# Kernel optimization log

Measured on AMD Instinct MI355X. Metric: run time of the kernel, lower is better.

The kernel has to match this reference:

```python
import jax, jax.numpy as jnp
import numpy as np

N, D, E = 50000, 128, 800000
BN_EPS = 1e-3  # keras BatchNormalization default


def _ffn_block(x, g, b, m, v, W, bias):
    # BatchNorm (inference) -> Dropout (identity at inference) -> Dense + exact GELU
    xn = (x - m) * g * jax.lax.rsqrt(v + BN_EPS) + b
    return jax.nn.gelu(xn @ W + bias, approximate=False)


def setup_inputs() -> dict:
    key = jax.random.key(0)
    ks = jax.random.split(key, 24)
    inp = {
        "node_reps": jax.random.normal(ks[0], (N, D), dtype=jnp.float32),
        "edges": jax.random.randint(ks[1], (2, E), 0, N, dtype=jnp.int32),
        "edge_weights": jax.random.uniform(ks[2], (E,), dtype=jnp.float32),
    }
    def bn(i, dim):
        return (jax.random.normal(ks[i], (dim,)) * 0.1 + 1.0,   # gamma
                jax.random.normal(ks[i + 1], (dim,)) * 0.1,      # beta
                jax.random.normal(ks[i + 2], (dim,)) * 0.1,      # moving mean
                jax.random.uniform(ks[i + 3], (dim,)) + 0.5)     # moving var (>0)
    # prepare FFN: two blocks, D->D then D->D
    inp["pre_bn1_g"], inp["pre_bn1_b"], inp["pre_bn1_m"], inp["pre_bn1_v"] = bn(3, D)
    inp["pre_w1"] = jax.random.normal(ks[7], (D, D)) * (1.0 / np.sqrt(D))
    inp["pre_b1"] = jnp.zeros((D,), jnp.float32)
    inp["pre_bn2_g"], inp["pre_bn2_b"], inp["pre_bn2_m"], inp["pre_bn2_v"] = bn(8, D)
    inp["pre_w2"] = jax.random.normal(ks[12], (D, D)) * (1.0 / np.sqrt(D))
    inp["pre_b2"] = jnp.zeros((D,), jnp.float32)
    # update FFN: concat -> 2D input, then D->D
    inp["upd_bn1_g"], inp["upd_bn1_b"], inp["upd_bn1_m"], inp["upd_bn1_v"] = bn(13, 2 * D)
    inp["upd_w1"] = jax.random.normal(ks[17], (2 * D, D)) * (1.0 / np.sqrt(2 * D))
    inp["upd_b1"] = jnp.zeros((D,), jnp.float32)
    inp["upd_bn2_g"], inp["upd_bn2_b"], inp["upd_bn2_m"], inp["upd_bn2_v"] = bn(18, D)
    inp["upd_w2"] = jax.random.normal(ks[22], (D, D)) * (1.0 / np.sqrt(D))
    inp["upd_b2"] = jnp.zeros((D,), jnp.float32)
    return inp


def reference(node_reps, edges, edge_weights,
              pre_bn1_g, pre_bn1_b, pre_bn1_m, pre_bn1_v, pre_w1, pre_b1,
              pre_bn2_g, pre_bn2_b, pre_bn2_m, pre_bn2_v, pre_w2, pre_b2,
              upd_bn1_g, upd_bn1_b, upd_bn1_m, upd_bn1_v, upd_w1, upd_b1,
              upd_bn2_g, upd_bn2_b, upd_bn2_m, upd_bn2_v, upd_w2, upd_b2):
    num_nodes = node_reps.shape[0]
    node_idx, nbr_idx = edges[0], edges[1]
    # gather neighbour representations [E, D]
    nbr = jnp.take(node_reps, nbr_idx, axis=0)
    # prepare: FFN then scale by edge weights
    msg = _ffn_block(nbr, pre_bn1_g, pre_bn1_b, pre_bn1_m, pre_bn1_v, pre_w1, pre_b1)
    msg = _ffn_block(msg, pre_bn2_g, pre_bn2_b, pre_bn2_m, pre_bn2_v, pre_w2, pre_b2)
    msg = msg * edge_weights[:, None]
    # aggregate: segment_sum scatter back to nodes [N, D]
    agg = jax.ops.segment_sum(msg, node_idx, num_segments=num_nodes)
    # update: concat + FFN, then L2 normalize
    h = jnp.concatenate([node_reps, agg], axis=-1)  # [N, 2D]
    out = _ffn_block(h, upd_bn1_g, upd_bn1_b, upd_bn1_m, upd_bn1_v, upd_w1, upd_b1)
    out = _ffn_block(out, upd_bn2_g, upd_bn2_b, upd_bn2_m, upd_bn2_v, upd_w2, upd_b2)
    out = out * jax.lax.rsqrt(jnp.maximum(jnp.sum(out * out, axis=-1, keepdims=True), 1e-12))
    return out
```

## Files before the change

kernel.cpp:

```cpp
#include <hip/hip_runtime.h>
#include <hip/hip_bf16.h>
#include <math.h>

#define NN 50000
#define DD 128
#define EE 800000

static constexpr float BN_EPS = 1e-3f;

typedef __attribute__((ext_vector_type(8))) short bf16x8;
typedef __attribute__((ext_vector_type(4))) float f32x4;

#define MFMA16(a, b, c) __builtin_amdgcn_mfma_f32_16x16x32_bf16((a), (b), (c), 0, 0, 0)

__device__ __forceinline__ float gelu_f(float x) {
    float ax = fabsf(x) * 0.7071067811865475f;
    float t = __builtin_amdgcn_rcpf(fmaf(0.3275911f, ax, 1.0f));
    float p = t * fmaf(t, fmaf(t, fmaf(t, fmaf(t, 1.061405429f, -1.453152027f),
                                       1.421413741f), -0.284496736f), 0.254829592f);
    float e = __expf(-ax * ax);
    float er = fmaf(-p, e, 1.0f);
    float s = copysignf(er, x);
    return 0.5f * x * (1.0f + s);
}

__device__ __forceinline__ ushort f2bf_rn(float f) {
    uint u = __float_as_uint(f);
    return (ushort)((u + 0x7FFFu + ((u >> 16) & 1u)) >> 16);
}
__device__ __forceinline__ float bf2f(ushort h) {
    return __uint_as_float(((uint)h) << 16);
}

__device__ __forceinline__ uint pk2(float a, float b) {
    __hip_bfloat162 t = __float22bfloat162_rn(make_float2(a, b));
    uint r;
    __builtin_memcpy(&r, &t, 4);
    return r;
}

__device__ __forceinline__ void cvt_hilo(float4 x0, float4 x1, bf16x8& h, bf16x8& l) {
    float f[8] = {x0.x, x0.y, x0.z, x0.w, x1.x, x1.y, x1.z, x1.w};
    union U { uint u[4]; bf16x8 v; } uh, ul;
    #pragma unroll
    for (int j = 0; j < 4; ++j) {
        uint p = pk2(f[2 * j], f[2 * j + 1]);
        uh.u[j] = p;
        float h0 = __uint_as_float(p << 16);
        float h1 = __uint_as_float(p & 0xFFFF0000u);
        ul.u[j] = pk2(f[2 * j] - h0, f[2 * j + 1] - h1);
    }
    h = uh.v;
    l = ul.v;
}

__device__ __forceinline__ void pack_one(const float* __restrict__ W, const float* __restrict__ g,
                                         const float* __restrict__ v, ushort* __restrict__ hi,
                                         ushort* __restrict__ lo, int K, int idx) {
    int k = idx >> 7, col = idx & 127;
    float s = g[k] * rsqrtf(v[k] + BN_EPS);
    float f = s * W[idx];
    int S = K >> 5;
    int st = k >> 5, gq = (k >> 3) & 3, j = k & 7;
    int c = col >> 4, ln = (gq << 4) | (col & 15);
    int o = ((c * S + st) * 64 + ln) * 8 + j;
    ushort hb = f2bf_rn(f);
    hi[o] = hb;
    lo[o] = f2bf_rn(f - bf2f(hb));
}

__global__ void pack_all(
    const float* __restrict__ w1, const float* __restrict__ g1, const float* __restrict__ v1,
    ushort* __restrict__ W1h, ushort* __restrict__ W1l,
    const float* __restrict__ w2, const float* __restrict__ g2, const float* __restrict__ v2,
    ushort* __restrict__ W2h, ushort* __restrict__ W2l,
    const float* __restrict__ u1, const float* __restrict__ g3, const float* __restrict__ v3,
    ushort* __restrict__ U1h, ushort* __restrict__ U1l,
    const float* __restrict__ u2, const float* __restrict__ g4, const float* __restrict__ v4,
    ushort* __restrict__ U2h, ushort* __restrict__ U2l)
{
    int idx = blockIdx.x * 256 + threadIdx.x;
    if (idx < 16384)       pack_one(w1, g1, v1, W1h, W1l, 128, idx);
    else if (idx < 32768)  pack_one(w2, g2, v2, W2h, W2l, 128, idx - 16384);
    else if (idx < 65536)  pack_one(u1, g3, v3, U1h, U1l, 256, idx - 32768);
    else                   pack_one(u2, g4, v4, U2h, U2l, 128, idx - 65536);
}

__global__ void init_bias(const float* __restrict__ b1, const float* __restrict__ b2,
                          const float* __restrict__ ub1, const float* __restrict__ ub2,
                          float* __restrict__ B1f, float* __restrict__ B2f,
                          float* __restrict__ C1f, float* __restrict__ C2f) {
    int t = threadIdx.x;
    B1f[t] = b1[t]; B2f[t] = b2[t]; C1f[t] = ub1[t]; C2f[t] = ub2[t];
}

__global__ __launch_bounds__(256) void fold_all(
    const float* __restrict__ w1, const float* __restrict__ g1, const float* __restrict__ b1,
    const float* __restrict__ m1, const float* __restrict__ v1, float* __restrict__ B1f,
    const float* __restrict__ w2, const float* __restrict__ g2, const float* __restrict__ b2,
    const float* __restrict__ m2, const float* __restrict__ v2, float* __restrict__ B2f,
    const float* __restrict__ u1, const float* __restrict__ g3, const float* __restrict__ b3,
    const float* __restrict__ m3, const float* __restrict__ v3, float* __restrict__ C1f,
    const float* __restrict__ u2, const float* __restrict__ g4, const float* __restrict__ b4,
    const float* __restrict__ m4, const float* __restrict__ v4, float* __restrict__ C2f,
    int* __restrict__ cnt, int* __restrict__ spillCnt)
{
    for (int i = blockIdx.x * 256 + threadIdx.x; i < NN + 1; i += 20 * 256) {
        if (i < NN) cnt[i] = 0; else spillCnt[0] = 0;
    }

    const int rs = blockIdx.x * 32;
    const float *W, *g, *bb, *m, *v;
    float* bf;
    int k0;
    if (rs < 128)      { W = w1; g = g1; bb = b1; m = m1; v = v1; bf = B1f; k0 = rs; }
    else if (rs < 256) { W = w2; g = g2; bb = b2; m = m2; v = v2; bf = B2f; k0 = rs - 128; }
    else if (rs < 512) { W = u1; g = g3; bb = b3; m = m3; v = v3; bf = C1f; k0 = rs - 256; }
    else               { W = u2; g = g4; bb = b4; m = m4; v = v4; bf = C2f; k0 = rs - 512; }

    const int t = threadIdx.x, j = t & 127, h = t >> 7;
    float acc = 0.f;
    #pragma unroll
    for (int kk = 0; kk < 16; ++kk) {
        int k = k0 + h * 16 + kk;
        float s = g[k] * rsqrtf(v[k] + BN_EPS);
        float tt = bb[k] - m[k] * s;
        acc = fmaf(tt, W[k * DD + j], acc);
    }
    __shared__ float S[256];
    S[t] = acc;
    __syncthreads();
    if (h == 0) atomicAdd(&bf[j], S[j] + S[128 + j]);
}

#define YLD 136
#define BCAP 56
#define SPILL_CAP 100000
#define NCHUNK 400
#define CHSZ (EE / NCHUNK)
#define PSZ 6250
#define FILLB (NCHUNK * 8)

__global__ __launch_bounds__(512, 4) void prep_fill(
    const float* __restrict__ reps, const int* __restrict__ edges,
    const ushort* __restrict__ W1h, const ushort* __restrict__ W1l, const float* __restrict__ B1,
    const ushort* __restrict__ W2h, const ushort* __restrict__ W2l, const float* __restrict__ B2,
    ushort* __restrict__ msgN,
    int* __restrict__ cnt, int* __restrict__ spillCnt,
    int* __restrict__ spill, int* __restrict__ bucket)
{
    __shared__ ushort Yh[128 * YLD];

    if (blockIdx.x < FILLB) {
        const int part = blockIdx.x & 7;
        const int ch   = blockIdx.x >> 3;
        const int lo = part * PSZ, hi2 = lo + PSZ;
        const int base = ch * CHSZ;
        for (int i = threadIdx.x; i < CHSZ; i += 512) {
            int e = base + i;
            int d = edges[e];
            if (d >= lo && d < hi2) {
                int s = atomicAdd(&cnt[d], 1);
                if (s < BCAP) bucket[d * BCAP + s] = e;
                else { int sl = atomicAdd(spillCnt, 1); if (sl < SPILL_CAP) spill[sl] = e; }
            }
        }
        return;
    }

    const int pb = blockIdx.x - FILLB;
    if (pb >= 391) return;
    const int t = threadIdx.x;
    const int w = t >> 6, l = t & 63, lg = l >> 4, lr = l & 15;
    const int n0 = pb * 128;
    int n = n0 + w * 16 + lr;
    int nc = n < NN ? n : NN - 1;
    const float* src = reps + (size_t)nc * DD;

    float b1v[8], b2v[8];
    #pragma unroll
    for (int c = 0; c < 8; ++c) { b1v[c] = B1[c * 16 + lr]; b2v[c] = B2[c * 16 + lr]; }

    f32x4 acc[8];
    #pragma unroll
    for (int c = 0; c < 8; ++c) acc[c] = (f32x4)(0.f);

    #pragma unroll
    for (int s = 0; s < 4; ++s) {
        float4 x0 = *reinterpret_cast<const float4*>(src + s * 32 + lg * 8);
        float4 x1 = *reinterpret_cast<const float4*>(src + s * 32 + lg * 8 + 4);
        bf16x8 ah, al;
        cvt_hilo(x0, x1, ah, al);
        #pragma unroll
        for (int c = 0; c < 8; ++c) {
            bf16x8 bh = *reinterpret_cast<const bf16x8*>(W1h + (size_t)((c * 4 + s) * 64 + l) * 8);
            bf16x8 bl = *reinterpret_cast<const bf16x8*>(W1l + (size_t)((c * 4 + s) * 64 + l) * 8);
            acc[c] = MFMA16(al, bh, acc[c]);
            acc[c] = MFMA16(ah, bl, acc[c]);
            acc[c] = MFMA16(ah, bh, acc[c]);
        }
    }
    #pragma unroll
    for (int c = 0; c < 8; ++c) {
        #pragma unroll
        for (int i = 0; i < 4; ++i) {
            float yv = gelu_f(acc[c][i] + b1v[c]);
            Yh[(w * 16 + lg * 4 + i) * YLD + c * 16 + lr] = f2bf_rn(yv);
        }
    }

    #pragma unroll
    for (int c = 0; c < 8; ++c) acc[c] = (f32x4)(0.f);
    const ushort* yr = Yh + (w * 16 + lr) * YLD;
    #pragma unroll
    for (int s = 0; s < 4; ++s) {
        bf16x8 ah = *reinterpret_cast<const bf16x8*>(yr + s * 32 + lg * 8);
        #pragma unroll
        for (int c = 0; c < 8; ++c) {
            bf16x8 bh = *reinterpret_cast<const bf16x8*>(W2h + (size_t)((c * 4 + s) * 64 + l) * 8);
            bf16x8 bl = *reinterpret_cast<const bf16x8*>(W2l + (size_t)((c * 4 + s) * 64 + l) * 8);
            acc[c] = MFMA16(ah, bl, acc[c]);
            acc[c] = MFMA16(ah, bh, acc[c]);
        }
    }

    const int nrow = n0 + w * 16 + lg * 4;
    #pragma unroll
    for (int i = 0; i < 4; ++i) {
        if (nrow + i < NN) {
            #pragma unroll
            for (int c = 0; c < 8; ++c)
                msgN[(size_t)(nrow + i) * DD + c * 16 + lr] = f2bf_rn(gelu_f(acc[c][i] + b2v[c]));
        }
    }
}

__global__ __launch_bounds__(512, 8) void agg_node(
    const float* __restrict__ reps, const int* __restrict__ edges, const float* __restrict__ ew,
    const int* __restrict__ bucket, const int* __restrict__ cnt,
    const int* __restrict__ spillCnt, const int* __restrict__ spill,
    const ushort* __restrict__ msgN,
    const ushort* __restrict__ U1h, const ushort* __restrict__ U1l, const float* __restrict__ C1,
    const ushort* __restrict__ U2h, const ushort* __restrict__ U2l, const float* __restrict__ C2,
    float* __restrict__ out)
{
    __shared__ ushort aggL[64 * YLD];
    __shared__ ushort Yh[64 * YLD];
    __shared__ float ssqP[2][64];
    const int t = threadIdx.x;
    const int n0 = blockIdx.x * 64;

    {
        const int g = t >> 4, la = t & 15;
        const ushort* base = msgN + la * 8;
        #pragma unroll
        for (int it = 0; it < 2; ++it) {
            const int nl = g * 2 + it;
            const int node = n0 + nl;
            float acc[8] = {0.f, 0.f, 0.f, 0.f, 0.f, 0.f, 0.f, 0.f};
            if (node < NN) {
                const int dc = cnt[node];
                const int deg = dc < BCAP ? dc : BCAP;
                const int* b = bucket + node * BCAP;
                int k = 0;
                for (; k + 3 < deg; k += 4) {
                    int e0 = b[k], e1 = b[k + 1], e2 = b[k + 2], e3 = b[k + 3];
                    int q0 = edges[EE + e0], q1 = edges[EE + e1];
                    int q2 = edges[EE + e2], q3 = edges[EE + e3];
                    float w0 = ew[e0], w1 = ew[e1], w2 = ew[e2], w3 = ew[e3];
                    bf16x8 m0 = *reinterpret_cast<const bf16x8*>(base + (size_t)q0 * DD);
                    bf16x8 m1 = *reinterpret_cast<const bf16x8*>(base + (size_t)q1 * DD);
                    bf16x8 m2 = *reinterpret_cast<const bf16x8*>(base + (size_t)q2 * DD);
                    bf16x8 m3 = *reinterpret_cast<const bf16x8*>(base + (size_t)q3 * DD);
                    #pragma unroll
                    for (int j = 0; j < 8; ++j) {
                        acc[j] = fmaf(w0, bf2f((ushort)m0[j]), acc[j]);
                        acc[j] = fmaf(w1, bf2f((ushort)m1[j]), acc[j]);
                        acc[j] = fmaf(w2, bf2f((ushort)m2[j]), acc[j]);
                        acc[j] = fmaf(w3, bf2f((ushort)m3[j]), acc[j]);
                    }
                }
                for (; k < deg; ++k) {
                    int e0 = b[k];
                    int q0 = edges[EE + e0];
                    float w0 = ew[e0];
                    bf16x8 m0 = *reinterpret_cast<const bf16x8*>(base + (size_t)q0 * DD);
                    #pragma unroll
                    for (int j = 0; j < 8; ++j) acc[j] = fmaf(w0, bf2f((ushort)m0[j]), acc[j]);
                }
                if (dc > BCAP) {
                    int sc = spillCnt[0]; if (sc > SPILL_CAP) sc = SPILL_CAP;
                    for (int i = 0; i < sc; ++i) {
                        int eid = spill[i];
                        if (edges[eid] == node) {
                            int q0 = edges[EE + eid];
                            float w0 = ew[eid];
                            bf16x8 m0 = *reinterpret_cast<const bf16x8*>(base + (size_t)q0 * DD);
                            #pragma unroll
                            for (int j = 0; j < 8; ++j)
                                acc[j] = fmaf(w0, bf2f((ushort)m0[j]), acc[j]);
                        }
                    }
                }
            }
            uint4 o;
            o.x = pk2(acc[0], acc[1]);
            o.y = pk2(acc[2], acc[3]);
            o.z = pk2(acc[4], acc[5]);
            o.w = pk2(acc[6], acc[7]);
            *reinterpret_cast<uint4*>(&aggL[nl * YLD + la * 8]) = o;
        }
    }
    __syncthreads();

    const int w = t >> 6, l = t & 63, lg = l >> 4, lr = l & 15;
    const int wr = w & 3, hh = w >> 2;
    int n = n0 + wr * 16 + lr;
    int nc = n < NN ? n : NN - 1;

    float c1v[4], c2v[4];
    #pragma unroll
    for (int cc = 0; cc < 4; ++cc) {
        c1v[cc] = C1[(4 * hh + cc) * 16 + lr];
        c2v[cc] = C2[(4 * hh + cc) * 16 + lr];
    }

    f32x4 acc[4];
    #pragma unroll
    for (int cc = 0; cc < 4; ++cc) acc[cc] = (f32x4)(0.f);

    #pragma unroll
    for (int s = 0; s < 4; ++s) {
        const float* sp = reps + (size_t)nc * DD + s * 32 + lg * 8;
        float4 x0 = *reinterpret_cast<const float4*>(sp);
        float4 x1 = *reinterpret_cast<const float4*>(sp + 4);
        bf16x8 ah, al;
        cvt_hilo(x0, x1, ah, al);
        #pragma unroll
        for (int cc = 0; cc < 4; ++cc) {
            int c = 4 * hh + cc;
            bf16x8 bh = *reinterpret_cast<const bf16x8*>(U1h + (size_t)((c * 8 + s) * 64 + l) * 8);
            bf16x8 bl = *reinterpret_cast<const bf16x8*>(U1l + (size_t)((c * 8 + s) * 64 + l) * 8);
            acc[cc] = MFMA16(al, bh, acc[cc]);
            acc[cc] = MFMA16(ah, bl, acc[cc]);
            acc[cc] = MFMA16(ah, bh, acc[cc]);
        }
    }
    const ushort* ar = aggL + (wr * 16 + lr) * YLD;
    #pragma unroll
    for (int s = 4; s < 8; ++s) {
        bf16x8 ah = *reinterpret_cast<const bf16x8*>(ar + (s - 4) * 32 + lg * 8);
        #pragma unroll
        for (int cc = 0; cc < 4; ++cc) {
            int c = 4 * hh + cc;
            bf16x8 bh = *reinterpret_cast<const bf16x8*>(U1h + (size_t)((c * 8 + s) * 64 + l) * 8);
            bf16x8 bl = *reinterpret_cast<const bf16x8*>(U1l + (size_t)((c * 8 + s) * 64 + l) * 8);
            acc[cc] = MFMA16(ah, bl, acc[cc]);
            acc[cc] = MFMA16(ah, bh, acc[cc]);
        }
    }
    #pragma unroll
    for (int cc = 0; cc < 4; ++cc) {
        #pragma unroll
        for (int i = 0; i < 4; ++i) {
            float yv = gelu_f(acc[cc][i] + c1v[cc]);
            Yh[(wr * 16 + lg * 4 + i) * YLD + (4 * hh + cc) * 16 + lr] = f2bf_rn(yv);
        }
    }
    __syncthreads();

    #pragma unroll
    for (int cc = 0; cc < 4; ++cc) acc[cc] = (f32x4)(0.f);
    const ushort* yr2 = Yh + (wr * 16 + lr) * YLD;
    #pragma unroll
    for (int s = 0; s < 4; ++s) {
        bf16x8 ah = *reinterpret_cast<const bf16x8*>(yr2 + s * 32 + lg * 8);
        #pragma unroll
        for (int cc = 0; cc < 4; ++cc) {
            int c = 4 * hh + cc;
            bf16x8 bh = *reinterpret_cast<const bf16x8*>(U2h + (size_t)((c * 4 + s) * 64 + l) * 8);
            bf16x8 bl = *reinterpret_cast<const bf16x8*>(U2l + (size_t)((c * 4 + s) * 64 + l) * 8);
            acc[cc] = MFMA16(ah, bl, acc[cc]);
            acc[cc] = MFMA16(ah, bh, acc[cc]);
        }
    }

    float ssq[4] = {0.f, 0.f, 0.f, 0.f};
    #pragma unroll
    for (int cc = 0; cc < 4; ++cc) {
        #pragma unroll
        for (int i = 0; i < 4; ++i) {
            float vv = gelu_f(acc[cc][i] + c2v[cc]);
            acc[cc][i] = vv;
            ssq[i] = fmaf(vv, vv, ssq[i]);
        }
    }
    #pragma unroll
    for (int i = 0; i < 4; ++i) {
        #pragma unroll
        for (int msk = 1; msk < 16; msk <<= 1) ssq[i] += __shfl_xor(ssq[i], msk);
    }
    const int row0 = wr * 16 + lg * 4;
    if (lr == 0) {
        #pragma unroll
        for (int i = 0; i < 4; ++i) ssqP[hh][row0 + i] = ssq[i];
    }
    __syncthreads();
    #pragma unroll
    for (int i = 0; i < 4; ++i) {
        float tot = ssqP[0][row0 + i] + ssqP[1][row0 + i];
        float sc = rsqrtf(fmaxf(tot, 1e-12f));
        if (n0 + row0 + i < NN) {
            #pragma unroll
            for (int cc = 0; cc < 4; ++cc)
                out[(size_t)(n0 + row0 + i) * DD + (4 * hh + cc) * 16 + lr] = acc[cc][i] * sc;
        }
    }
}

extern "C" void kernel_launch(void* const* d_in, const int* in_sizes, int n_in,
                              void* d_out, int out_size, void* d_ws, size_t ws_size,
                              hipStream_t stream)
{
    const float* reps = (const float*)d_in[0];
    const int*   edges = (const int*)d_in[1];
    const float* ew   = (const float*)d_in[2];
    const float* bn1g = (const float*)d_in[3];
    const float* bn1b = (const float*)d_in[4];
    const float* bn1m = (const float*)d_in[5];
    const float* bn1v = (const float*)d_in[6];
    const float* w1   = (const float*)d_in[7];
    const float* b1   = (const float*)d_in[8];
    const float* bn2g = (const float*)d_in[9];
    const float* bn2b = (const float*)d_in[10];
    const float* bn2m = (const float*)d_in[11];
    const float* bn2v = (const float*)d_in[12];
    const float* w2   = (const float*)d_in[13];
    const float* b2   = (const float*)d_in[14];
    const float* ubn1g = (const float*)d_in[15];
    const float* ubn1b = (const float*)d_in[16];
    const float* ubn1m = (const float*)d_in[17];
    const float* ubn1v = (const float*)d_in[18];
    const float* u1    = (const float*)d_in[19];
    const float* ub1   = (const float*)d_in[20];
    const float* ubn2g = (const float*)d_in[21];
    const float* ubn2b = (const float*)d_in[22];
    const float* ubn2m = (const float*)d_in[23];
    const float* ubn2v = (const float*)d_in[24];
    const float* u2    = (const float*)d_in[25];
    const float* ub2   = (const float*)d_in[26];

    char* wsb = (char*)d_ws;
    ushort* msgN     = (ushort*)wsb;
    int*    bucket   = (int*)(wsb + 12800000);
    int*    cnt      = (int*)(wsb + 24000000);
    int*    spillCnt = (int*)(wsb + 24200000);
    int*    spill    = (int*)(wsb + 24200016);
    float*  B1f      = (float*)(wsb + 24600016);
    float*  B2f = B1f + 128;
    float*  C1f = B2f + 128;
    float*  C2f = C1f + 128;
    ushort* up  = (ushort*)(C2f + 128);
    ushort* W1h = up;
    ushort* W1l = W1h + 16384;
    ushort* W2h = W1l + 16384;
    ushort* W2l = W2h + 16384;
    ushort* U1h = W2l + 16384;
    ushort* U1l = U1h + 32768;
    ushort* U2h = U1l + 32768;
    ushort* U2l = U2h + 16384;
    if (ws_size < 24950000) return;

    init_bias<<<1, 128, 0, stream>>>(b1, b2, ub1, ub2, B1f, B2f, C1f, C2f);
    pack_all<<<320, 256, 0, stream>>>(w1, bn1g, bn1v, W1h, W1l,
                                      w2, bn2g, bn2v, W2h, W2l,
                                      u1, ubn1g, ubn1v, U1h, U1l,
                                      u2, ubn2g, ubn2v, U2h, U2l);
    fold_all<<<20, 256, 0, stream>>>(w1, bn1g, bn1b, bn1m, bn1v, B1f,
                                     w2, bn2g, bn2b, bn2m, bn2v, B2f,
                                     u1, ubn1g, ubn1b, ubn1m, ubn1v, C1f,
                                     u2, ubn2g, ubn2b, ubn2m, ubn2v, C2f,
                                     cnt, spillCnt);

    prep_fill<<<FILLB + 392, 512, 0, stream>>>(reps, edges, W1h, W1l, B1f,
                                               W2h, W2l, B2f, msgN,
                                               cnt, spillCnt, spill, bucket);
    agg_node<<<(NN + 63) / 64, 512, 0, stream>>>(reps, edges, ew, bucket, cnt,
                                                 spillCnt, spill, msgN,
                                                 U1h, U1l, C1f, U2h, U2l, C2f,
                                                 (float*)d_out);
}
```

Measured before the change: 161.7 us.

## Shrink agg_node blocks to 16 nodes with 256 threads

Restructures the aggregation+update kernel so each block handles 16 nodes with 4 waves instead of 64 nodes with 8 waves. Each thread now gathers one node instead of two, and each wave computes 32 output columns for all 16 rows instead of 64 columns for 16 rows. This gives 3125 blocks instead of 782, aiming at better load balance across CUs and more parallel gather latency hiding, at the cost of reloading the U1/U2 weights more often per node and more blocks overall. Bounds checks are dropped because NN divides evenly by 16.

```diff
diff --git a/kernel.cpp b/kernel.cpp
--- a/kernel.cpp
+++ b/kernel.cpp
@@ -235,7 +235,7 @@
     }
 }
 
-__global__ __launch_bounds__(512, 8) void agg_node(
+__global__ __launch_bounds__(256, 8) void agg_node(
     const float* __restrict__ reps, const int* __restrict__ edges, const float* __restrict__ ew,
     const int* __restrict__ bucket, const int* __restrict__ cnt,
     const int* __restrict__ spillCnt, const int* __restrict__ spill,
@@ -244,101 +244,92 @@
     const ushort* __restrict__ U2h, const ushort* __restrict__ U2l, const float* __restrict__ C2,
     float* __restrict__ out)
 {
-    __shared__ ushort aggL[64 * YLD];
-    __shared__ ushort Yh[64 * YLD];
-    __shared__ float ssqP[2][64];
+    __shared__ ushort aggL[16 * YLD];
+    __shared__ ushort Yh[16 * YLD];
+    __shared__ float ssqP[4][16];
     const int t = threadIdx.x;
-    const int n0 = blockIdx.x * 64;
+    const int n0 = blockIdx.x * 16;
 
     {
         const int g = t >> 4, la = t & 15;
+        const int node = n0 + g;
         const ushort* base = msgN + la * 8;
-        #pragma unroll
-        for (int it = 0; it < 2; ++it) {
-            const int nl = g * 2 + it;
-            const int node = n0 + nl;
-            float acc[8] = {0.f, 0.f, 0.f, 0.f, 0.f, 0.f, 0.f, 0.f};
-            if (node < NN) {
-                const int dc = cnt[node];
-                const int deg = dc < BCAP ? dc : BCAP;
-                const int* b = bucket + node * BCAP;
-                int k = 0;
-                for (; k + 3 < deg; k += 4) {
-                    int e0 = b[k], e1 = b[k + 1], e2 = b[k + 2], e3 = b[k + 3];
-                    int q0 = edges[EE + e0], q1 = edges[EE + e1];
-                    int q2 = edges[EE + e2], q3 = edges[EE + e3];
-                    float w0 = ew[e0], w1 = ew[e1], w2 = ew[e2], w3 = ew[e3];
-                    bf16x8 m0 = *reinterpret_cast<const bf16x8*>(base + (size_t)q0 * DD);
-                    bf16x8 m1 = *reinterpret_cast<const bf16x8*>(base + (size_t)q1 * DD);
-                    bf16x8 m2 = *reinterpret_cast<const bf16x8*>(base + (size_t)q2 * DD);
-                    bf16x8 m3 = *reinterpret_cast<const bf16x8*>(base + (size_t)q3 * DD);
-                    #pragma unroll
-                    for (int j = 0; j < 8; ++j) {
-                        acc[j] = fmaf(w0, bf2f((ushort)m0[j]), acc[j]);
-                        acc[j] = fmaf(w1, bf2f((ushort)m1[j]), acc[j]);
-                        acc[j] = fmaf(w2, bf2f((ushort)m2[j]), acc[j]);
-                        acc[j] = fmaf(w3, bf2f((ushort)m3[j]), acc[j]);
-                    }
-                }
-                for (; k < deg; ++k) {
-                    int e0 = b[k];
-                    int q0 = edges[EE + e0];
-                    float w0 = ew[e0];
+        float acc[8] = {0.f, 0.f, 0.f, 0.f, 0.f, 0.f, 0.f, 0.f};
+        const int dc = cnt[node];
+        const int deg = dc < BCAP ? dc : BCAP;
+        const int* b = bucket + node * BCAP;
+        int k = 0;
+        for (; k + 3 < deg; k += 4) {
+            int e0 = b[k], e1 = b[k + 1], e2 = b[k + 2], e3 = b[k + 3];
+            int q0 = edges[EE + e0], q1 = edges[EE + e1];
+            int q2 = edges[EE + e2], q3 = edges[EE + e3];
+            float w0 = ew[e0], w1 = ew[e1], w2 = ew[e2], w3 = ew[e3];
+            bf16x8 m0 = *reinterpret_cast<const bf16x8*>(base + (size_t)q0 * DD);
+            bf16x8 m1 = *reinterpret_cast<const bf16x8*>(base + (size_t)q1 * DD);
+            bf16x8 m2 = *reinterpret_cast<const bf16x8*>(base + (size_t)q2 * DD);
+            bf16x8 m3 = *reinterpret_cast<const bf16x8*>(base + (size_t)q3 * DD);
+            #pragma unroll
+            for (int j = 0; j < 8; ++j) {
+                acc[j] = fmaf(w0, bf2f((ushort)m0[j]), acc[j]);
+                acc[j] = fmaf(w1, bf2f((ushort)m1[j]), acc[j]);
+                acc[j] = fmaf(w2, bf2f((ushort)m2[j]), acc[j]);
+                acc[j] = fmaf(w3, bf2f((ushort)m3[j]), acc[j]);
+            }
+        }
+        for (; k < deg; ++k) {
+            int e0 = b[k];
+            int q0 = edges[EE + e0];
+            float w0 = ew[e0];
+            bf16x8 m0 = *reinterpret_cast<const bf16x8*>(base + (size_t)q0 * DD);
+            #pragma unroll
+            for (int j = 0; j < 8; ++j) acc[j] = fmaf(w0, bf2f((ushort)m0[j]), acc[j]);
+        }
+        if (dc > BCAP) {
+            int sc = spillCnt[0]; if (sc > SPILL_CAP) sc = SPILL_CAP;
+            for (int i = 0; i < sc; ++i) {
+                int eid = spill[i];
+                if (edges[eid] == node) {
+                    int q0 = edges[EE + eid];
+                    float w0 = ew[eid];
                     bf16x8 m0 = *reinterpret_cast<const bf16x8*>(base + (size_t)q0 * DD);
                     #pragma unroll
-                    for (int j = 0; j < 8; ++j) acc[j] = fmaf(w0, bf2f((ushort)m0[j]), acc[j]);
-                }
-                if (dc > BCAP) {
-                    int sc = spillCnt[0]; if (sc > SPILL_CAP) sc = SPILL_CAP;
-                    for (int i = 0; i < sc; ++i) {
-                        int eid = spill[i];
-                        if (edges[eid] == node) {
-                            int q0 = edges[EE + eid];
-                            float w0 = ew[eid];
-                            bf16x8 m0 = *reinterpret_cast<const bf16x8*>(base + (size_t)q0 * DD);
-                            #pragma unroll
-                            for (int j = 0; j < 8; ++j)
-                                acc[j] = fmaf(w0, bf2f((ushort)m0[j]), acc[j]);
-                        }
-                    }
+                    for (int j = 0; j < 8; ++j)
+                        acc[j] = fmaf(w0, bf2f((ushort)m0[j]), acc[j]);
                 }
             }
-            uint4 o;
-            o.x = pk2(acc[0], acc[1]);
-            o.y = pk2(acc[2], acc[3]);
-            o.z = pk2(acc[4], acc[5]);
-            o.w = pk2(acc[6], acc[7]);
-            *reinterpret_cast<uint4*>(&aggL[nl * YLD + la * 8]) = o;
-        }
+        }
+        uint4 o;
+        o.x = pk2(acc[0], acc[1]);
+        o.y = pk2(acc[2], acc[3]);
+        o.z = pk2(acc[4], acc[5]);
+        o.w = pk2(acc[6], acc[7]);
+        *reinterpret_cast<uint4*>(&aggL[g * YLD + la * 8]) = o;
     }
     __syncthreads();
 
     const int w = t >> 6, l = t & 63, lg = l >> 4, lr = l & 15;
-    const int wr = w & 3, hh = w >> 2;
-    int n = n0 + wr * 16 + lr;
-    int nc = n < NN ? n : NN - 1;
-
-    float c1v[4], c2v[4];
-    #pragma unroll
-    for (int cc = 0; cc < 4; ++cc) {
-        c1v[cc] = C1[(4 * hh + cc) * 16 + lr];
-        c2v[cc] = C2[(4 * hh + cc) * 16 + lr];
-    }
-
-    f32x4 acc[4];
-    #pragma unroll
-    for (int cc = 0; cc < 4; ++cc) acc[cc] = (f32x4)(0.f);
+
+    float c1v[2], c2v[2];
+    #pragma unroll
+    for (int cc = 0; cc < 2; ++cc) {
+        c1v[cc] = C1[(2 * w + cc) * 16 + lr];
+        c2v[cc] = C2[(2 * w + cc) * 16 + lr];
+    }
+
+    f32x4 acc[2];
+    #pragma unroll
+    for (int cc = 0; cc < 2; ++cc) acc[cc] = (f32x4)(0.f);
 
     #pragma unroll
     for (int s = 0; s < 4; ++s) {
-        const float* sp = reps + (size_t)nc * DD + s * 32 + lg * 8;
+        const float* sp = reps + (size_t)(n0 + lr) * DD + s * 32 + lg * 8;
         float4 x0 = *reinterpret_cast<const float4*>(sp);
         float4 x1 = *reinterpret_cast<const float4*>(sp + 4);
         bf16x8 ah, al;
         cvt_hilo(x0, x1, ah, al);
         #pragma unroll
-        for (int cc = 0; cc < 4; ++cc) {
-            int c = 4 * hh + cc;
+        for (int cc = 0; cc < 2; ++cc) {
+            int c = 2 * w + cc;
             bf16x8 bh = *reinterpret_cast<const bf16x8*>(U1h + (size_t)((c * 8 + s) * 64 + l) * 8);
             bf16x8 bl = *reinterpret_cast<const bf16x8*>(U1l + (size_t)((c * 8 + s) * 64 + l) * 8);
             acc[cc] = MFMA16(al, bh, acc[cc]);
@@ -346,13 +337,13 @@
             acc[cc] = MFMA16(ah, bh, acc[cc]);
         }
     }
-    const ushort* ar = aggL + (wr * 16 + lr) * YLD;
+    const ushort* ar = aggL + lr * YLD;
     #pragma unroll
     for (int s = 4; s < 8; ++s) {
         bf16x8 ah = *reinterpret_cast<const bf16x8*>(ar + (s - 4) * 32 + lg * 8);
         #pragma unroll
-        for (int cc = 0; cc < 4; ++cc) {
-            int c = 4 * hh + cc;
+        for (int cc = 0; cc < 2; ++cc) {
+            int c = 2 * w + cc;
             bf16x8 bh = *reinterpret_cast<const bf16x8*>(U1h + (size_t)((c * 8 + s) * 64 + l) * 8);
             bf16x8 bl = *reinterpret_cast<const bf16x8*>(U1l + (size_t)((c * 8 + s) * 64 + l) * 8);
             acc[cc] = MFMA16(ah, bl, acc[cc]);
@@ -360,24 +351,24 @@
         }
     }
     #pragma unroll
-    for (int cc = 0; cc < 4; ++cc) {
+    for (int cc = 0; cc < 2; ++cc) {
         #pragma unroll
         for (int i = 0; i < 4; ++i) {
             float yv = gelu_f(acc[cc][i] + c1v[cc]);
-            Yh[(wr * 16 + lg * 4 + i) * YLD + (4 * hh + cc) * 16 + lr] = f2bf_rn(yv);
+            Yh[(lg * 4 + i) * YLD + (2 * w + cc) * 16 + lr] = f2bf_rn(yv);
         }
     }
     __syncthreads();
 
     #pragma unroll
-    for (int cc = 0; cc < 4; ++cc) acc[cc] = (f32x4)(0.f);
-    const ushort* yr2 = Yh + (wr * 16 + lr) * YLD;
+    for (int cc = 0; cc < 2; ++cc) acc[cc] = (f32x4)(0.f);
+    const ushort* yr2 = Yh + lr * YLD;
     #pragma unroll
     for (int s = 0; s < 4; ++s) {
         bf16x8 ah = *reinterpret_cast<const bf16x8*>(yr2 + s * 32 + lg * 8);
         #pragma unroll
-        for (int cc = 0; cc < 4; ++cc) {
-            int c = 4 * hh + cc;
+        for (int cc = 0; cc < 2; ++cc) {
+            int c = 2 * w + cc;
             bf16x8 bh = *reinterpret_cast<const bf16x8*>(U2h + (size_t)((c * 4 + s) * 64 + l) * 8);
             bf16x8 bl = *reinterpret_cast<const bf16x8*>(U2l + (size_t)((c * 4 + s) * 64 + l) * 8);
             acc[cc] = MFMA16(ah, bl, acc[cc]);
@@ -387,7 +378,7 @@
 
     float ssq[4] = {0.f, 0.f, 0.f, 0.f};
     #pragma unroll
-    for (int cc = 0; cc < 4; ++cc) {
+    for (int cc = 0; cc < 2; ++cc) {
         #pragma unroll
         for (int i = 0; i < 4; ++i) {
             float vv = gelu_f(acc[cc][i] + c2v[cc]);
@@ -400,21 +391,20 @@
         #pragma unroll
         for (int msk = 1; msk < 16; msk <<= 1) ssq[i] += __shfl_xor(ssq[i], msk);
     }
-    const int row0 = wr * 16 + lg * 4;
+    const int row0 = lg * 4;
     if (lr == 0) {
         #pragma unroll
-        for (int i = 0; i < 4; ++i) ssqP[hh][row0 + i] = ssq[i];
+        for (int i = 0; i < 4; ++i) ssqP[w][row0 + i] = ssq[i];
     }
     __syncthreads();
     #pragma unroll
     for (int i = 0; i < 4; ++i) {
-        float tot = ssqP[0][row0 + i] + ssqP[1][row0 + i];
+        float tot = ssqP[0][row0 + i] + ssqP[1][row0 + i] +
+                    ssqP[2][row0 + i] + ssqP[3][row0 + i];
         float sc = rsqrtf(fmaxf(tot, 1e-12f));
-        if (n0 + row0 + i < NN) {
-            #pragma unroll
-            for (int cc = 0; cc < 4; ++cc)
-                out[(size_t)(n0 + row0 + i) * DD + (4 * hh + cc) * 16 + lr] = acc[cc][i] * sc;
-        }
+        #pragma unroll
+        for (int cc = 0; cc < 2; ++cc)
+            out[(size_t)(n0 + row0 + i) * DD + (2 * w + cc) * 16 + lr] = acc[cc][i] * sc;
     }
 }
 
@@ -485,8 +475,8 @@
     prep_fill<<<FILLB + 392, 512, 0, stream>>>(reps, edges, W1h, W1l, B1f,
                                                W2h, W2l, B2f, msgN,
                                                cnt, spillCnt, spill, bucket);
-    agg_node<<<(NN + 63) / 64, 512, 0, stream>>>(reps, edges, ew, bucket, cnt,
-                                                 spillCnt, spill, msgN,
-                                                 U1h, U1l, C1f, U2h, U2l, C2f,
-                                                 (float*)d_out);
-}
+    agg_node<<<NN / 16, 256, 0, stream>>>(reps, edges, ew, bucket, cnt,
+                                          spillCnt, spill, msgN,
+                                          U1h, U1l, C1f, U2h, U2l, C2f,
+                                          (float*)d_out);
+}
```

Result: faster. 155.8 us (-3.7%).
